# Optimization experiments

Measured on AMD Instinct MI355X. Metric: run time of the kernel, lower is better.

## Reference

```python
import jax, jax.numpy as jnp
import numpy as np

N_SRC0, N_DST0, N_DST1 = 400000, 200000, 100000
E0, E1 = 3200000, 1600000
IN_FEATS, H_FEATS, NUM_CLASSES, NUM_CELL_TYPES = 128, 256, 8, 24


def setup_inputs() -> dict:
    key = jax.random.key(0)
    ks = jax.random.split(key, 12)
    feats = jax.random.normal(ks[0], (N_SRC0, IN_FEATS), dtype=jnp.float32)
    cell_ids = jax.random.randint(ks[1], (N_SRC0,), 0, NUM_CELL_TYPES)
    x = jnp.concatenate([cell_ids.astype(jnp.float32)[:, None], feats], axis=1)  # [N,129]
    src0 = jax.random.randint(ks[2], (E0,), 0, N_SRC0, dtype=jnp.int32)
    dst0 = jax.random.randint(ks[3], (E0,), 0, N_DST0, dtype=jnp.int32)
    src1 = jax.random.randint(ks[4], (E1,), 0, N_DST0, dtype=jnp.int32)
    dst1 = jax.random.randint(ks[5], (E1,), 0, N_DST1, dtype=jnp.int32)
    s = 1.0 / np.sqrt(IN_FEATS)
    s2 = 1.0 / np.sqrt(H_FEATS)
    return {
        "x": x,
        "src0": src0, "dst0": dst0, "src1": src1, "dst1": dst1,
        "n_dst0": N_DST0, "n_dst1": N_DST1,
        "emb": jax.random.normal(ks[6], (NUM_CELL_TYPES, IN_FEATS), dtype=jnp.float32),
        "W_self1": jax.random.normal(ks[7], (IN_FEATS, H_FEATS), dtype=jnp.float32) * s,
        "W_neigh1": jax.random.normal(ks[8], (IN_FEATS, H_FEATS), dtype=jnp.float32) * s,
        "b1": jnp.zeros((H_FEATS,), dtype=jnp.float32),
        "W_self2": jax.random.normal(ks[9], (H_FEATS, NUM_CLASSES), dtype=jnp.float32) * s2,
        "W_neigh2": jax.random.normal(ks[10], (H_FEATS, NUM_CLASSES), dtype=jnp.float32) * s2,
        "b2": jnp.zeros((NUM_CLASSES,), dtype=jnp.float32),
    }


def _sage_mean(h_src, h_dst, src, dst, n_dst, W_self, W_neigh, b):
    # gather src features along edges, mean-reduce onto dst nodes
    msg = h_src[src]                                                # [E, d]
    agg = jax.ops.segment_sum(msg, dst, num_segments=n_dst)        # [n_dst, d]
    deg = jax.ops.segment_sum(jnp.ones_like(dst, dtype=h_src.dtype), dst, num_segments=n_dst)
    agg = agg / jnp.maximum(deg, 1.0)[:, None]
    return h_dst @ W_self + agg @ W_neigh + b


def reference(x, src0, dst0, src1, dst1, n_dst0, n_dst1,
              emb, W_self1, W_neigh1, b1, W_self2, W_neigh2, b2):
    cell_ids = x[:, 0].astype(jnp.int32)
    feat = x[:, 1:]
    h = feat * jax.nn.sigmoid(emb[cell_ids])  # embedding-gated features; dropout = identity (eval)
    h_dst = h[:n_dst0]
    h1 = jax.nn.relu(_sage_mean(h, h_dst, src0, dst0, n_dst0, W_self1, W_neigh1, b1))
    h1_dst = h1[:n_dst1]
    out = _sage_mean(h1, h1_dst, src1, dst1, n_dst1, W_self2, W_neigh2, b2)
    return out
```

## Files before the change

kernel.cpp:

```cpp
#include <hip/hip_runtime.h>

typedef unsigned int uint;
typedef unsigned short ushort;
typedef __attribute__((ext_vector_type(8))) short short8;
typedef __attribute__((ext_vector_type(4))) float f32x4;

__device__ __forceinline__ float bflo(uint u) { return __uint_as_float(u << 16); }
__device__ __forceinline__ float bfhi(uint u) { return __uint_as_float(u & 0xffff0000u); }
__device__ __forceinline__ ushort f2bf(float f) {
    uint u = __float_as_uint(f);
    u += 0x7fffu + ((u >> 16) & 1u);
    return (ushort)(u >> 16);
}
__device__ __forceinline__ uint pack2(float a, float b) {
    return (uint)f2bf(a) | ((uint)f2bf(b) << 16);
}
__device__ __forceinline__ float sigm(float e) { return 1.0f / (1.0f + __expf(-e)); }

#define ND0 200000
#define ND1 100000
#define INF 128
#define HF  256
#define BCAP 32768
#define GSTRIDE 16
#define NBKT 200
#define CAP_A 48
#define SENT 0xFFFFFFFFu

__global__ __launch_bounds__(256) void gate_k(const float* __restrict__ x,
                                              const float* __restrict__ emb,
                                              ushort* __restrict__ h, int nnodes) {
    int tid  = blockIdx.x * 256 + threadIdx.x;
    int node = tid >> 4, tq = tid & 15;
    if (node >= nnodes) return;
    const float* xr = x + (size_t)node * 129;
    int cell = (int)xr[0];
    int f0 = tq * 8;
    const float* er = emb + cell * INF + f0;
    float4 e0 = *(const float4*)er;
    float4 e1 = *(const float4*)(er + 4);
    float v[8];
    __builtin_memcpy(&v[0], xr + 1 + f0, 16);
    __builtin_memcpy(&v[4], xr + 5 + f0, 16);
    uint4 o;
    o.x = pack2(v[0] * sigm(e0.x), v[1] * sigm(e0.y));
    o.y = pack2(v[2] * sigm(e0.z), v[3] * sigm(e0.w));
    o.z = pack2(v[4] * sigm(e1.x), v[5] * sigm(e1.y));
    o.w = pack2(v[6] * sigm(e1.z), v[7] * sigm(e1.w));
    *(uint4*)(h + (size_t)node * INF + f0) = o;
}

#define SCAN_B 1024
__global__ __launch_bounds__(256) void scan1_k(const int* __restrict__ in,
                                               int* __restrict__ out,
                                               int* __restrict__ bsum, int n) {
    __shared__ int tmp[256];
    int t = threadIdx.x;
    int base = blockIdx.x * SCAN_B;
    int v[4], s = 0;
#pragma unroll
    for (int q = 0; q < 4; ++q) {
        int idx = base + t * 4 + q;
        v[q] = (idx < n) ? ((in[idx] + 3) & ~3) : 0;
        s += v[q];
    }
    tmp[t] = s; __syncthreads();
    for (int off = 1; off < 256; off <<= 1) {
        int xv = (t >= off) ? tmp[t - off] : 0; __syncthreads();
        tmp[t] += xv; __syncthreads();
    }
    int excl = tmp[t] - s;
#pragma unroll
    for (int q = 0; q < 4; ++q) {
        int idx = base + t * 4 + q;
        if (idx < n) out[idx] = excl;
        excl += v[q];
    }
    if (t == 255) bsum[blockIdx.x] = tmp[255];
}

__global__ __launch_bounds__(256) void scan2_k(int* __restrict__ bsum, int nb) {
    __shared__ int tmp[256];
    int t = threadIdx.x;
    int s = (t < nb) ? bsum[t] : 0;
    tmp[t] = s; __syncthreads();
    for (int off = 1; off < 256; off <<= 1) {
        int xv = (t >= off) ? tmp[t - off] : 0; __syncthreads();
        tmp[t] += xv; __syncthreads();
    }
    if (t < nb) bsum[t] = tmp[t] - s;
}

__global__ __launch_bounds__(256) void scan3_k(int* __restrict__ row_start,
                                               const int* __restrict__ bsum, int n) {
    int i = blockIdx.x * blockDim.x + threadIdx.x;
    if (i < n) row_start[i] += bsum[i >> 10];
}

template <int CPT>
__global__ __launch_bounds__(256) void binA_k(const int* __restrict__ src,
                                              const int* __restrict__ dst,
                                              uint* __restrict__ pairs,
                                              int* __restrict__ gcur, int E) {
    __shared__ int  lcur[NBKT];
    __shared__ uint stage[NBKT][CAP_A];
    int t = threadIdx.x;
    int c0 = blockIdx.x * (256 * CPT);
    int n = min(256 * CPT, E - c0);
    for (int i = t; i < NBKT; i += 256) lcur[i] = 0;
    __syncthreads();

    int i0 = t * CPT;
    if (i0 + CPT <= n) {
#pragma unroll
        for (int v = 0; v < CPT / 4; ++v) {
            int4 d4 = *(const int4*)(dst + c0 + i0 + v * 4);
            int4 s4 = *(const int4*)(src + c0 + i0 + v * 4);
            int dv[4] = { d4.x, d4.y, d4.z, d4.w };
            int sv[4] = { s4.x, s4.y, s4.z, s4.w };
#pragma unroll
            for (int q = 0; q < 4; ++q) {
                int d = dv[q];
                int b = d >> 10;
                uint e = ((uint)sv[q] << 10) | (uint)(d & 1023);
                int r = atomicAdd(&lcur[b], 1);
                if (r < CAP_A) stage[b][r] = e;
                else {
                    int p = atomicAdd(&gcur[b * GSTRIDE], 1);
                    pairs[(size_t)b * BCAP + p] = e;
                }
            }
        }
    } else {
        for (int q = 0; q < CPT; ++q) {
            int i = i0 + q;
            if (i >= n) break;
            int d = dst[c0 + i];
            int b = d >> 10;
            uint e = ((uint)src[c0 + i] << 10) | (uint)(d & 1023);
            int r = atomicAdd(&lcur[b], 1);
            if (r < CAP_A) stage[b][r] = e;
            else {
                int p = atomicAdd(&gcur[b * GSTRIDE], 1);
                pairs[(size_t)b * BCAP + p] = e;
            }
        }
    }
    __syncthreads();

    int wid = t >> 6, lane = t & 63;
    for (int b = wid; b < NBKT; b += 4) {
        int cnt = min(lcur[b], CAP_A);
        if (cnt == 0) continue;
        int padded = (cnt + 15) & ~15;
        int base;
        if (lane == 0) base = atomicAdd(&gcur[b * GSTRIDE], padded);
        base = __shfl(base, 0);
        if (lane < padded)
            pairs[(size_t)b * BCAP + base + lane] = (lane < cnt) ? stage[b][lane] : SENT;
    }
}

__global__ __launch_bounds__(1024) void binC_k(const uint* __restrict__ pairs,
                                               const int* __restrict__ gcur,
                                               int* __restrict__ cnt, int nd) {
    __shared__ int h[1024];
    int b = blockIdx.x, t = threadIdx.x;
    h[t] = 0;
    __syncthreads();
    int ne = gcur[b * GSTRIDE];
    const uint* bp = pairs + (size_t)b * BCAP;
    for (int i = t; i < ne; i += 1024) {
        uint e = bp[i];
        if (e != SENT) atomicAdd(&h[e & 1023], 1);
    }
    __syncthreads();
    int d = (b << 10) + t;
    if (d < nd) cnt[d] = h[t];
}

__global__ __launch_bounds__(1024) void binB_k(const uint* __restrict__ pairs,
                                               const int* __restrict__ gcur,
                                               const int* __restrict__ row_start,
                                               int* __restrict__ csr, int nd, int zrow) {
    __shared__ int cur[1024];
    int b = blockIdx.x, t = threadIdx.x;
    int dbase = b << 10;
    cur[t] = (dbase + t < nd) ? row_start[dbase + t] : 0;
    __syncthreads();
    int ne = gcur[b * GSTRIDE];
    const uint* bp = pairs + (size_t)b * BCAP;
    for (int i = t; i < ne; i += 1024) {
        uint e = bp[i];
        if (e == SENT) continue;
        int p = atomicAdd(&cur[e & 1023], 1);
        csr[p] = (int)(e >> 10);
    }
    __syncthreads();
    if (dbase + t < nd) {
        int pe = cur[t];
        int pad = (-(pe - row_start[dbase + t])) & 3;
        for (int q = 0; q < pad; ++q) csr[pe + q] = zrow;
    }
}

__global__ __launch_bounds__(256) void gather4_k(const int* __restrict__ csr,
                                                 const int* __restrict__ row_start,
                                                 const int* __restrict__ cnt,
                                                 const ushort* __restrict__ hsrc,
                                                 uint* __restrict__ aggm, int nrows) {
    int w    = (blockIdx.x * blockDim.x + threadIdx.x) >> 6;
    int lane = threadIdx.x & 63;
    if (w >= nrows) return;
    int beg = row_start[w], c = cnt[w];
    int end = beg + ((c + 3) & ~3);
    const uint* hb = (const uint*)hsrc;
    float a0 = 0.f, a1 = 0.f;
    for (int j = beg; j < end; j += 4) {
        int4 s4 = *(const int4*)(csr + j);
        uint u0 = hb[(size_t)s4.x * 64 + lane];
        uint u1 = hb[(size_t)s4.y * 64 + lane];
        uint u2 = hb[(size_t)s4.z * 64 + lane];
        uint u3 = hb[(size_t)s4.w * 64 + lane];
        a0 += (bflo(u0) + bflo(u1)) + (bflo(u2) + bflo(u3));
        a1 += (bfhi(u0) + bfhi(u1)) + (bfhi(u2) + bfhi(u3));
    }
    float inv = 1.0f / fmaxf((float)c, 1.0f);
    aggm[(size_t)w * 64 + lane] = pack2(a0 * inv, a1 * inv);
}

__global__ __launch_bounds__(256) void wconv_k(const float* __restrict__ Ws,
                                               const float* __restrict__ Wn,
                                               uint* __restrict__ Wb) {
    int tid  = blockIdx.x * 256 + threadIdx.x;
    int lane = tid & 63, nf = (tid >> 6) & 15, ks = tid >> 10;
    int n  = nf * 16 + (lane & 15);
    int k0 = ks * 32 + ((lane >> 4) << 3);
    uint o[4];
#pragma unroll
    for (int p = 0; p < 4; ++p) {
        int k = k0 + 2 * p;
        float a = (k < 128)     ? Ws[(size_t)k * HF + n]       : Wn[(size_t)(k - 128) * HF + n];
        float b = (k + 1 < 128) ? Ws[(size_t)(k + 1) * HF + n] : Wn[(size_t)(k - 127) * HF + n];
        o[p] = pack2(a, b);
    }
    uint4 v = { o[0], o[1], o[2], o[3] };
    *(uint4*)(Wb + (size_t)tid * 4) = v;
}

__global__ __launch_bounds__(256) void wpack2_k(const float* __restrict__ Ws2,
                                                const float* __restrict__ Wn2,
                                                uint* __restrict__ Wb2) {
    int tid = blockIdx.x * 256 + threadIdx.x;
    if (tid >= 512) return;
    int lane = tid & 63, ks = tid >> 6;
    int n  = lane & 15;
    int k0 = ks * 32 + ((lane >> 4) << 3);
    const float* W = (n < 8) ? Wn2 : Ws2;
    int c = n & 7;
    uint o[4];
#pragma unroll
    for (int p = 0; p < 4; ++p) {
        int k = k0 + 2 * p;
        o[p] = pack2(W[(size_t)k * 8 + c], W[(size_t)(k + 1) * 8 + c]);
    }
    uint4 v = { o[0], o[1], o[2], o[3] };
    *(uint4*)(Wb2 + (size_t)tid * 4) = v;
}

__global__ __launch_bounds__(256) void layer1_mfma_k(const uint* __restrict__ hb,
                                                     const uint* __restrict__ aggm,
                                                     const uint* __restrict__ Wb,
                                                     const uint* __restrict__ Wb2,
                                                     const float* __restrict__ b1,
                                                     float* __restrict__ z,
                                                     float* __restrict__ out, int nd1) {
    __shared__ uint lds[64 * 132];
    int t = threadIdx.x, lane = t & 63, wid = t >> 6;
    int quad = lane >> 4, l16 = lane & 15;
    int r0 = blockIdx.x * 64;

#pragma unroll
    for (int it = 0; it < 8; ++it) {
        int i = t + it * 256;
        int r = i >> 5, u4 = i & 31;
        const uint* src = (u4 < 16) ? (hb + (size_t)(r0 + r) * 64 + u4 * 4)
                                    : (aggm + (size_t)(r0 + r) * 64 + (u4 - 16) * 4);
        *(uint4*)&lds[r * 132 + u4 * 4] = *(const uint4*)src;
    }

    float bias[4];
#pragma unroll
    for (int i = 0; i < 4; ++i) bias[i] = b1[wid * 64 + i * 16 + l16];
    f32x4 acc[4][4];
#pragma unroll
    for (int mf = 0; mf < 4; ++mf)
#pragma unroll
        for (int i = 0; i < 4; ++i)
            acc[mf][i] = (f32x4){ bias[i], bias[i], bias[i], bias[i] };

    __syncthreads();

#pragma unroll
    for (int ks = 0; ks < 8; ++ks) {
        short8 bfr[4];
#pragma unroll
        for (int i = 0; i < 4; ++i) {
            int nf = wid * 4 + i;
            bfr[i] = *(const short8*)(Wb + (size_t)((ks * 16 + nf) * 64 + lane) * 4);
        }
        short8 afr[4];
#pragma unroll
        for (int mf = 0; mf < 4; ++mf) {
            int r = mf * 16 + l16;
            afr[mf] = *(const short8*)&lds[r * 132 + ks * 16 + quad * 4];
        }
#pragma unroll
        for (int mf = 0; mf < 4; ++mf)
#pragma unroll
            for (int i = 0; i < 4; ++i)
                acc[mf][i] = __builtin_amdgcn_mfma_f32_16x16x32_bf16(afr[mf], bfr[i],
                                                                     acc[mf][i], 0, 0, 0);
    }

    __syncthreads();
    ushort* st = (ushort*)lds;
#pragma unroll
    for (int mf = 0; mf < 4; ++mf)
#pragma unroll
        for (int i = 0; i < 4; ++i) {
            int col = wid * 64 + i * 16 + l16;
#pragma unroll
            for (int reg = 0; reg < 4; ++reg) {
                int row = mf * 16 + quad * 4 + reg;
                st[row * 264 + col] = f2bf(fmaxf(acc[mf][i][reg], 0.0f));
            }
        }
    __syncthreads();

    f32x4 zacc = (f32x4){ 0.f, 0.f, 0.f, 0.f };
    int rloc = wid * 16 + l16;
#pragma unroll
    for (int ks = 0; ks < 8; ++ks) {
        short8 a = *(const short8*)&lds[rloc * 132 + ks * 16 + quad * 4];
        short8 b = *(const short8*)(Wb2 + (size_t)(ks * 64 + lane) * 4);
        zacc = __builtin_amdgcn_mfma_f32_16x16x32_bf16(a, b, zacc, 0, 0, 0);
    }
#pragma unroll
    for (int reg = 0; reg < 4; ++reg) {
        int r = r0 + wid * 16 + quad * 4 + reg;
        if (l16 < 8) z[(size_t)r * 8 + l16] = zacc[reg];
        else if (r < nd1) out[(size_t)r * 8 + (l16 - 8)] = zacc[reg];
    }
}

__global__ __launch_bounds__(256) void gz_k(const int* __restrict__ csr,
                                            const int* __restrict__ row_start,
                                            const int* __restrict__ cnt,
                                            const float* __restrict__ z,
                                            const float* __restrict__ b2,
                                            float* __restrict__ out, int nrows) {
    int tid = blockIdx.x * 256 + threadIdx.x;
    int d = tid >> 3, c = tid & 7;
    if (d >= nrows) return;
    int beg = row_start[d], n = cnt[d];
    int end = beg + ((n + 3) & ~3);
    float a = 0.f;
    for (int j = beg; j < end; j += 4) {
        int4 s4 = *(const int4*)(csr + j);
        a += z[(size_t)s4.x * 8 + c] + z[(size_t)s4.y * 8 + c]
           + z[(size_t)s4.z * 8 + c] + z[(size_t)s4.w * 8 + c];
    }
    float inv = 1.0f / fmaxf((float)n, 1.0f);
    out[(size_t)d * 8 + c] += a * inv + b2[c];
}

extern "C" void kernel_launch(void* const* d_in, const int* in_sizes, int n_in,
                              void* d_out, int out_size, void* d_ws, size_t ws_size,
                              hipStream_t stream) {
    const float* x    = (const float*)d_in[0];
    const int*   src0 = (const int*)d_in[1];
    const int*   dst0 = (const int*)d_in[2];
    const int*   src1 = (const int*)d_in[3];
    const int*   dst1 = (const int*)d_in[4];
    const float* emb  = (const float*)d_in[7];
    const float* Ws1  = (const float*)d_in[8];
    const float* Wn1  = (const float*)d_in[9];
    const float* b1   = (const float*)d_in[10];
    const float* Ws2  = (const float*)d_in[11];
    const float* Wn2  = (const float*)d_in[12];
    const float* b2   = (const float*)d_in[13];
    int E0 = in_sizes[1];
    int E1 = in_sizes[3];
    int nsrc = in_sizes[0] / 129;

    char* p = (char*)d_ws;
    ushort* h         = (ushort*)p;  p += ((size_t)nsrc + 1) * INF * 2;
    uint*   aggm      = (uint*)p;    p += (size_t)ND0 * 64 * 4;
    int*    csr       = (int*)p;     p += ((size_t)E0 + 3 * (size_t)ND0 + 16) * 4;
    int*    cnt       = (int*)p;     p += (size_t)ND0 * 4;
    int*    row_start = (int*)p;     p += (size_t)ND0 * 4;
    int*    bsum      = (int*)p;     p += 256 * 4;
    int*    gcur      = (int*)p;     p += 256 * GSTRIDE * 4;
    uint*   Wb        = (uint*)p;    p += 8192 * 16;
    uint*   Wb2       = (uint*)p;    p += 512 * 16;
    float*  z         = (float*)p;   p += ((size_t)ND0 + 1) * 8 * 4;
    uint*   pairs     = aggm;

    int ZR0 = nsrc;
    int ZR1 = ND0;

    hipMemsetAsync(gcur, 0, 256 * GSTRIDE * 4, stream);
    hipMemsetAsync(h + (size_t)ZR0 * INF, 0, INF * 2, stream);
    gate_k<<<(nsrc * 16 + 255) / 256, 256, 0, stream>>>(x, emb, h, nsrc);
    wconv_k<<<32, 256, 0, stream>>>(Ws1, Wn1, Wb);
    wpack2_k<<<2, 256, 0, stream>>>(Ws2, Wn2, Wb2);
    int nb0 = (ND0 + SCAN_B - 1) / SCAN_B;
    int ch0 = (E0 + 256 * 16 - 1) / (256 * 16);
    binA_k<16><<<ch0, 256, 0, stream>>>(src0, dst0, pairs, gcur, E0);
    binC_k<<<nb0, 1024, 0, stream>>>(pairs, gcur, cnt, ND0);
    scan1_k<<<nb0, 256, 0, stream>>>(cnt, row_start, bsum, ND0);
    scan2_k<<<1, 256, 0, stream>>>(bsum, nb0);
    scan3_k<<<(ND0 + 255) / 256, 256, 0, stream>>>(row_start, bsum, ND0);
    binB_k<<<nb0, 1024, 0, stream>>>(pairs, gcur, row_start, csr, ND0, ZR0);
    gather4_k<<<(ND0 + 3) / 4, 256, 0, stream>>>(csr, row_start, cnt, h, aggm, ND0);
    layer1_mfma_k<<<ND0 / 64, 256, 0, stream>>>((const uint*)h, aggm, Wb, Wb2, b1,
                                                z, (float*)d_out, ND1);

    hipMemsetAsync(gcur, 0, 256 * GSTRIDE * 4, stream);
    hipMemsetAsync(z + (size_t)ZR1 * 8, 0, 8 * 4, stream);
    int nb1 = (ND1 + SCAN_B - 1) / SCAN_B;
    int ch1 = (E1 + 256 * 8 - 1) / (256 * 8);
    binA_k<8><<<ch1, 256, 0, stream>>>(src1, dst1, pairs, gcur, E1);
    binC_k<<<nb1, 1024, 0, stream>>>(pairs, gcur, cnt, ND1);
    scan1_k<<<nb1, 256, 0, stream>>>(cnt, row_start, bsum, ND1);
    scan2_k<<<1, 256, 0, stream>>>(bsum, nb1);
    scan3_k<<<(ND1 + 255) / 256, 256, 0, stream>>>(row_start, bsum, ND1);
    binB_k<<<nb1, 1024, 0, stream>>>(pairs, gcur, row_start, csr, ND1, ZR1);
    gz_k<<<(ND1 * 8 + 255) / 256, 256, 0, stream>>>(csr, row_start, cnt, z, b2,
                                                    (float*)d_out, ND1);
}
```

Measured before the change: 733.4 us.

## Widen gather loads to 16B per lane with quarter-wave edge split and prefetch

The layer-1 gather now splits each wavefront into four 16-lane groups. Each group handles one of four edges per step and loads 16 bytes of the bf16 row per lane instead of 4, then the partial sums are combined with xor shuffles. CSR indices are software-prefetched one iteration ahead in both gather kernels, and bin pair reads use nontemporal loads. The goal is fewer, wider memory transactions and hidden index-load latency, at the cost of extra cross-lane shuffles and more register use.

Measured after the change: 762.3 us. 1.04x slower.

```diff
diff --git a/kernel.cpp b/kernel.cpp
--- a/kernel.cpp
+++ b/kernel.cpp
@@ -171,7 +171,7 @@
     int ne = gcur[b * GSTRIDE];
     const uint* bp = pairs + (size_t)b * BCAP;
     for (int i = t; i < ne; i += 1024) {
-        uint e = bp[i];
+        uint e = __builtin_nontemporal_load(bp + i);
         if (e != SENT) atomicAdd(&h[e & 1023], 1);
     }
     __syncthreads();
@@ -191,7 +191,7 @@
     int ne = gcur[b * GSTRIDE];
     const uint* bp = pairs + (size_t)b * BCAP;
     for (int i = t; i < ne; i += 1024) {
-        uint e = bp[i];
+        uint e = __builtin_nontemporal_load(bp + i);
         if (e == SENT) continue;
         int p = atomicAdd(&cur[e & 1023], 1);
         csr[p] = (int)(e >> 10);
@@ -212,21 +212,39 @@
     int w    = (blockIdx.x * blockDim.x + threadIdx.x) >> 6;
     int lane = threadIdx.x & 63;
     if (w >= nrows) return;
+    int e  = lane >> 4;
+    int fo = (lane & 15) * 4;
     int beg = row_start[w], c = cnt[w];
     int end = beg + ((c + 3) & ~3);
     const uint* hb = (const uint*)hsrc;
-    float a0 = 0.f, a1 = 0.f;
-    for (int j = beg; j < end; j += 4) {
-        int4 s4 = *(const int4*)(csr + j);
-        uint u0 = hb[(size_t)s4.x * 64 + lane];
-        uint u1 = hb[(size_t)s4.y * 64 + lane];
-        uint u2 = hb[(size_t)s4.z * 64 + lane];
-        uint u3 = hb[(size_t)s4.w * 64 + lane];
-        a0 += (bflo(u0) + bflo(u1)) + (bflo(u2) + bflo(u3));
-        a1 += (bfhi(u0) + bfhi(u1)) + (bfhi(u2) + bfhi(u3));
-    }
-    float inv = 1.0f / fmaxf((float)c, 1.0f);
-    aggm[(size_t)w * 64 + lane] = pack2(a0 * inv, a1 * inv);
+    float a[8] = {0.f, 0.f, 0.f, 0.f, 0.f, 0.f, 0.f, 0.f};
+    if (beg < end) {
+        int r = __builtin_nontemporal_load(csr + beg + e);
+        for (int j = beg; j < end; j += 4) {
+            int rn = 0;
+            if (j + 4 < end) rn = __builtin_nontemporal_load(csr + j + 4 + e);
+            uint4 hv = *(const uint4*)(hb + (size_t)r * 64 + fo);
+            a[0] += bflo(hv.x); a[1] += bfhi(hv.x);
+            a[2] += bflo(hv.y); a[3] += bfhi(hv.y);
+            a[4] += bflo(hv.z); a[5] += bfhi(hv.z);
+            a[6] += bflo(hv.w); a[7] += bfhi(hv.w);
+            r = rn;
+        }
+    }
+#pragma unroll
+    for (int i = 0; i < 8; ++i) {
+        a[i] += __shfl_xor(a[i], 16);
+        a[i] += __shfl_xor(a[i], 32);
+    }
+    if (lane < 16) {
+        float inv = 1.0f / fmaxf((float)c, 1.0f);
+        uint4 o;
+        o.x = pack2(a[0] * inv, a[1] * inv);
+        o.y = pack2(a[2] * inv, a[3] * inv);
+        o.z = pack2(a[4] * inv, a[5] * inv);
+        o.w = pack2(a[6] * inv, a[7] * inv);
+        *(uint4*)(aggm + (size_t)w * 64 + fo) = o;
+    }
 }
 
 __global__ __launch_bounds__(256) void wconv_k(const float* __restrict__ Ws,
@@ -366,10 +384,15 @@
     int beg = row_start[d], n = cnt[d];
     int end = beg + ((n + 3) & ~3);
     float a = 0.f;
-    for (int j = beg; j < end; j += 4) {
-        int4 s4 = *(const int4*)(csr + j);
-        a += z[(size_t)s4.x * 8 + c] + z[(size_t)s4.y * 8 + c]
-           + z[(size_t)s4.z * 8 + c] + z[(size_t)s4.w * 8 + c];
+    if (beg < end) {
+        int4 s4 = *(const int4*)(csr + beg);
+        for (int j = beg; j < end; j += 4) {
+            int4 nx = {0, 0, 0, 0};
+            if (j + 4 < end) nx = *(const int4*)(csr + j + 4);
+            a += z[(size_t)s4.x * 8 + c] + z[(size_t)s4.y * 8 + c]
+               + z[(size_t)s4.z * 8 + c] + z[(size_t)s4.w * 8 + c];
+            s4 = nx;
+        }
     }
     float inv = 1.0f / fmaxf((float)n, 1.0f);
     out[(size_t)d * 8 + c] += a * inv + b2[c];
```
